# Kernel tuning notes

Hardware: AMD Instinct MI355X
Metric: run time of the kernel (lower is better)

The kernel has to match this reference:

```python
import jax, jax.numpy as jnp
import numpy as np

EMB = 128  # embsize
WORD = 128  # word_size
ITERS = 2


def _agg(embeds, neibors):
    # embeds: [B, N, D], neibors: [B, N, K] indices into node axis N (per batch)
    # mean-pool gathered neighbor embeddings -> [B, N, D]
    gathered = jax.vmap(lambda e, idx: e[idx])(embeds, neibors)  # [B, N, K, D]
    return gathered.mean(axis=2)


def setup_inputs() -> dict:
    key = jax.random.key(0)
    ks = jax.random.split(key, 9)
    B, N, K = 64, 512, 16
    word_embs = jax.random.normal(ks[0], (B, N, WORD), dtype=jnp.float32)
    lib_embs = jax.random.normal(ks[1], (B, N, WORD), dtype=jnp.float32)
    neibors = jax.random.randint(ks[2], (B, N, K), 0, N)
    neibors_lib = jax.random.randint(ks[3], (B, N, K), 0, N)
    mask = jax.random.uniform(ks[4], (B, N), dtype=jnp.float32)
    # xavier-uniform style params
    def xav(k, shape):
        bound = float(np.sqrt(6.0 / (shape[0] + shape[1])))
        return jax.random.uniform(k, shape, dtype=jnp.float32, minval=-bound, maxval=bound)
    weight = xav(ks[5], (WORD, EMB))
    weight2 = xav(ks[6], (EMB, EMB))
    enc_w1 = xav(ks[7], (WORD, EMB))
    enc_w2 = xav(ks[8], (EMB, EMB))
    return {"word_embs": word_embs, "neibors": neibors, "lib_embs": lib_embs,
            "neibors_lib": neibors_lib, "mask": mask, "weight": weight,
            "weight2": weight2, "enc_w1": enc_w1, "enc_w2": enc_w2}


def reference(word_embs, neibors, lib_embs, neibors_lib, mask, weight, weight2, enc_w1, enc_w2):
    B, N, _ = word_embs.shape
    # lib aggregation is loop-invariant (lib_embs fixed); same math as in-loop recompute
    agg_lib = jnp.einsum('bnw,we->bne', _agg(lib_embs, neibors_lib), weight)  # [B, N, EMB]
    word_proj = jnp.einsum('bnw,we->bne', word_embs, enc_w1)  # loop-invariant
    last_embed = jnp.zeros((B, N, EMB), dtype=jnp.float32)
    for _ in range(ITERS):
        agg_func = _agg(last_embed, neibors)  # [B, N, EMB]
        last_embed = jnp.tanh(word_proj + jnp.einsum('bne,ef->bnf', agg_func, enc_w2) + agg_lib)
    # masked sum over nodes, then final linear
    pooled = (last_embed * mask[:, :, None]).sum(axis=1)  # [B, EMB]
    return pooled @ weight2
```

## Files before the change

### kernel.cpp

```cpp
#include <hip/hip_runtime.h>
#include <hip/hip_bf16.h>

#define B_   64
#define N_   512
#define D_   128
#define NPB  16
#define G1   ((B_*N_)/NPB)

typedef float f32x4  __attribute__((ext_vector_type(4)));
typedef _Float16 f16x8 __attribute__((ext_vector_type(8)));

static __device__ __forceinline__ unsigned pkrtz(float x, float y) {
    return __builtin_bit_cast(unsigned, __builtin_amdgcn_cvt_pkrtz(x, y));
}
static __device__ __forceinline__ short f2h(float x) {
    _Float16 h = (_Float16)x;
    return __builtin_bit_cast(short, h);
}
static __device__ __forceinline__ float h2f(short s) {
    return (float)__builtin_bit_cast(_Float16, s);
}
static __device__ __forceinline__ float fast_tanh(float x) {
    float e = __expf(2.f * x);
    return 1.f - 2.f * __builtin_amdgcn_rcpf(e + 1.f);
}
static __device__ __forceinline__ void pk_add16(unsigned& acc, unsigned v) {
    asm("v_pk_add_f16 %0, %1, %0" : "+v"(acc) : "v"(v));
}

__global__ __launch_bounds__(256) void prep(const float* __restrict__ lib,
                                            const float* __restrict__ enc1,
                                            const float* __restrict__ wgt,
                                            const float* __restrict__ enc2,
                                            short* __restrict__ libh,
                                            short* __restrict__ Bp1,
                                            short* __restrict__ Bp2,
                                            float* __restrict__ out) {
    const int blk = blockIdx.x;
    if (blk < 1024) {
        const size_t g = ((size_t)blk * 256 + threadIdx.x) * 16;
        unsigned o[8];
#pragma unroll
        for (int q = 0; q < 4; ++q) {
            float4 v = *(const float4*)&lib[g + q * 4];
            o[q * 2]     = pkrtz(v.x, v.y);
            o[q * 2 + 1] = pkrtz(v.z, v.w);
        }
        *(int4*)&libh[g]     = *(int4*)o;
        *(int4*)&libh[g + 8] = *(int4*)(o + 4);
        return;
    }
    int tid = (blk - 1024) * 256 + threadIdx.x;
    out[tid] = 0.f;
    short o8[8];
    if (tid < 4096) {
        int l = tid & 63, nt = (tid >> 6) & 7, ks = tid >> 9;
        int k0 = ks * 32 + (l >> 4) * 8;
        int col = nt * 16 + (l & 15);
#pragma unroll
        for (int j = 0; j < 8; ++j) {
            int r = k0 + j;
            float v = (r < 128) ? enc1[r * 128 + col] : wgt[(r - 128) * 128 + col] * 0.0625f;
            o8[j] = f2h(v);
        }
        *(int4*)&Bp1[(size_t)tid * 8] = *(int4*)o8;
    } else if (tid < 6144) {
        int t2 = tid - 4096;
        int l = t2 & 63, nt = (t2 >> 6) & 7, ks = t2 >> 9;
        int k0 = ks * 32 + (l >> 4) * 8;
        int col = nt * 16 + (l & 15);
#pragma unroll
        for (int j = 0; j < 8; ++j) o8[j] = f2h(enc2[(k0 + j) * 128 + col] * 0.0625f);
        *(int4*)&Bp2[(size_t)t2 * 8] = *(int4*)o8;
    }
}

static __device__ __forceinline__ int swz_blk() {
    const int hw = blockIdx.x;
    return ((hw & 7) << 8) + (hw >> 3);
}

#define LDA1 264
#define LDA2 136

__global__ __launch_bounds__(256) void gemm1(const float* __restrict__ word,
                                             const int* __restrict__ nbrL,
                                             const short* __restrict__ libh,
                                             const short* __restrict__ Bp1,
                                             short* __restrict__ baseh,
                                             short* __restrict__ t1) {
    __shared__ short sA[NPB * LDA1];
    __shared__ int sIdx[NPB * 16];
    const int tid = threadIdx.x;
    const int blk = swz_blk();
    const int b = blk >> 5;
    const int node0 = blk * NPB;

    if (tid < 64) *(int4*)&sIdx[tid * 4] = *(const int4*)&nbrL[(size_t)node0 * 16 + tid * 4];
    __syncthreads();

    const int row = tid >> 4;
    const int lg  = tid & 15;

    {
        const float* wr = word + (size_t)(node0 + row) * D_ + lg * 8;
        float4 v0 = *(const float4*)&wr[0];
        float4 v1 = *(const float4*)&wr[4];
        unsigned o[4] = { pkrtz(v0.x, v0.y), pkrtz(v0.z, v0.w),
                          pkrtz(v1.x, v1.y), pkrtz(v1.z, v1.w) };
        *(int4*)&sA[row * LDA1 + lg * 8] = *(int4*)o;
    }

    {
        int idxr[16];
#pragma unroll
        for (int q = 0; q < 4; ++q) *(int4*)&idxr[q * 4] = *(const int4*)&sIdx[row * 16 + q * 4];
        const char* libB = (const char*)libh + (size_t)b * N_ * D_ * 2 + lg * 16;
        unsigned a0 = 0, a1 = 0, a2 = 0, a3 = 0;
#pragma unroll
        for (int nb = 0; nb < 16; ++nb) {
            int4 d = *(const int4*)(libB + ((unsigned)idxr[nb] << 8));
            pk_add16(a0, (unsigned)d.x);
            pk_add16(a1, (unsigned)d.y);
            pk_add16(a2, (unsigned)d.z);
            pk_add16(a3, (unsigned)d.w);
        }
        unsigned o[4] = { a0, a1, a2, a3 };
        *(int4*)&sA[row * LDA1 + 128 + lg * 8] = *(int4*)o;
    }
    __syncthreads();

    const int w = tid >> 6, l = tid & 63;
    f32x4 acc[2];
    acc[0] = (f32x4)0.f; acc[1] = (f32x4)0.f;
    const int arow = l & 15;
#pragma unroll
    for (int ks = 0; ks < 8; ++ks) {
        f16x8 a = *(const f16x8*)&sA[arow * LDA1 + ks * 32 + (l >> 4) * 8];
#pragma unroll
        for (int j = 0; j < 2; ++j) {
            const int nt = 2 * w + j;
            f16x8 bb = *(const f16x8*)&Bp1[((size_t)(ks * 8 + nt) * 64 + l) * 8];
            acc[j] = __builtin_amdgcn_mfma_f32_16x16x32_f16(a, bb, acc[j], 0, 0, 0);
        }
    }

    const int r0 = (l >> 4) * 4;
    const int cl = l & 15;
#pragma unroll
    for (int j = 0; j < 2; ++j) {
        const int col = (2 * w + j) * 16 + cl;
#pragma unroll
        for (int r = 0; r < 4; ++r) {
            size_t o = (size_t)(node0 + r0 + r) * D_ + col;
            float v = acc[j][r];
            baseh[o] = f2h(v);
            t1[o]    = f2h(fast_tanh(v));
        }
    }
}

__global__ __launch_bounds__(256) void gemm2(const short* __restrict__ t1,
                                             const int* __restrict__ nbr,
                                             const short* __restrict__ Bp2,
                                             const short* __restrict__ baseh,
                                             const float* __restrict__ mask,
                                             const float* __restrict__ w2,
                                             float* __restrict__ out) {
    __shared__ short sA[NPB * LDA2];
    __shared__ int sIdx[NPB * 16];
    __shared__ float pred[128];
    __shared__ float smask[NPB];
    const int tid = threadIdx.x;
    const int blk = swz_blk();
    const int b = blk >> 5;
    const int node0 = blk * NPB;

    if (tid < 64) *(int4*)&sIdx[tid * 4] = *(const int4*)&nbr[(size_t)node0 * 16 + tid * 4];
    if (tid >= 64 && tid < 64 + NPB) smask[tid - 64] = mask[node0 + tid - 64];
    __syncthreads();

    const int row = tid >> 4;
    const int lg  = tid & 15;
    {
        int idxr[16];
#pragma unroll
        for (int q = 0; q < 4; ++q) *(int4*)&idxr[q * 4] = *(const int4*)&sIdx[row * 16 + q * 4];
        const char* tB = (const char*)t1 + (size_t)b * N_ * D_ * 2 + lg * 16;
        unsigned a0 = 0, a1 = 0, a2 = 0, a3 = 0;
#pragma unroll
        for (int nb = 0; nb < 16; ++nb) {
            int4 d = *(const int4*)(tB + ((unsigned)idxr[nb] << 8));
            pk_add16(a0, (unsigned)d.x);
            pk_add16(a1, (unsigned)d.y);
            pk_add16(a2, (unsigned)d.z);
            pk_add16(a3, (unsigned)d.w);
        }
        unsigned o[4] = { a0, a1, a2, a3 };
        *(int4*)&sA[row * LDA2 + lg * 8] = *(int4*)o;
    }
    __syncthreads();

    const int w = tid >> 6, l = tid & 63;
    f32x4 acc[2];
    acc[0] = (f32x4)0.f; acc[1] = (f32x4)0.f;
    const int arow = l & 15;
#pragma unroll
    for (int ks = 0; ks < 4; ++ks) {
        f16x8 a = *(const f16x8*)&sA[arow * LDA2 + ks * 32 + (l >> 4) * 8];
#pragma unroll
        for (int j = 0; j < 2; ++j) {
            const int nt = 2 * w + j;
            f16x8 bb = *(const f16x8*)&Bp2[((size_t)(ks * 8 + nt) * 64 + l) * 8];
            acc[j] = __builtin_amdgcn_mfma_f32_16x16x32_f16(a, bb, acc[j], 0, 0, 0);
        }
    }

    const int r0 = (l >> 4) * 4;
    const int cl = l & 15;
#pragma unroll
    for (int j = 0; j < 2; ++j) {
        const int col = (2 * w + j) * 16 + cl;
        float s = 0.f;
#pragma unroll
        for (int r = 0; r < 4; ++r) {
            size_t o = (size_t)(node0 + r0 + r) * D_ + col;
            float v = fast_tanh(h2f(baseh[o]) + acc[j][r]);
            s += v * smask[r0 + r];
        }
        s += __shfl_xor(s, 16);
        s += __shfl_xor(s, 32);
        if (l < 16) pred[col] = s;
    }
    __syncthreads();
    if (tid < 128) {
        float a2 = 0.f;
#pragma unroll 4
        for (int f = 0; f < 128; ++f) a2 += pred[f] * w2[f * 128 + tid];
        atomicAdd(&out[b * 128 + tid], a2);
    }
}

extern "C" void kernel_launch(void* const* d_in, const int* in_sizes, int n_in,
                              void* d_out, int out_size, void* d_ws, size_t ws_size,
                              hipStream_t stream) {
    const float* word_embs   = (const float*)d_in[0];
    const int*   neibors     = (const int*)d_in[1];
    const float* lib_embs    = (const float*)d_in[2];
    const int*   neibors_lib = (const int*)d_in[3];
    const float* mask        = (const float*)d_in[4];
    const float* weight      = (const float*)d_in[5];
    const float* weight2     = (const float*)d_in[6];
    const float* enc_w1      = (const float*)d_in[7];
    const float* enc_w2      = (const float*)d_in[8];
    float* out = (float*)d_out;

    char* ws = (char*)d_ws;
    short* baseh = (short*)(ws);
    short* t1    = (short*)(ws + (1u << 23));
    short* libh  = (short*)(ws + (2u << 23));
    short* Bp1   = (short*)(ws + (3u << 23));
    short* Bp2   = (short*)(ws + (3u << 23) + 65536);

    prep<<<1056, 256, 0, stream>>>(lib_embs, enc_w1, weight, enc_w2, libh, Bp1, Bp2, out);
    gemm1<<<G1, 256, 0, stream>>>(word_embs, neibors_lib, libh, Bp1, baseh, t1);
    gemm2<<<G1, 256, 0, stream>>>(t1, neibors, Bp2, baseh, mask, weight2, out);
}
```

Before: 48.29 us.

## Reorder aggregation and matmul; gather neighbors from LDS windows in separate kernels

Neighbor mean-aggregation is linear, so the second-iteration matmul by enc_w2 is applied per node before aggregating. That lets the first kernel produce both the base projection and u = tanh(base)·W2. Neighbor gathers move into dedicated kernels (aggL, aggU). Each one loads a per-batch, per-16-channel slice of all 512 nodes into shared memory and gathers from there instead of doing random global loads. The lib embeddings are stored channel-chunked for contiguous slice loads, and a final kernel applies tanh, mask pooling and the weight2 projection. This trades fewer scattered global reads for two extra launches and extra intermediate buffers written and read through global memory.

```diff
diff --git a/kernel.cpp b/kernel.cpp
--- a/kernel.cpp
+++ b/kernel.cpp
@@ -4,8 +4,6 @@
 #define B_   64
 #define N_   512
 #define D_   128
-#define NPB  16
-#define G1   ((B_*N_)/NPB)
 
 typedef float f32x4  __attribute__((ext_vector_type(4)));
 typedef _Float16 f16x8 __attribute__((ext_vector_type(8)));
@@ -32,22 +30,26 @@
                                             const float* __restrict__ enc1,
                                             const float* __restrict__ wgt,
                                             const float* __restrict__ enc2,
-                                            short* __restrict__ libh,
+                                            short* __restrict__ libc,
                                             short* __restrict__ Bp1,
                                             short* __restrict__ Bp2,
                                             float* __restrict__ out) {
     const int blk = blockIdx.x;
     if (blk < 1024) {
-        const size_t g = ((size_t)blk * 256 + threadIdx.x) * 16;
+        const int g = blk * 256 + threadIdx.x;
+        const int b = g >> 12, rem = g & 4095;
+        const int r = rem >> 3, ch = rem & 7;
+        const float* src = lib + ((size_t)(b * 512 + r)) * 128 + ch * 16;
         unsigned o[8];
 #pragma unroll
         for (int q = 0; q < 4; ++q) {
-            float4 v = *(const float4*)&lib[g + q * 4];
+            float4 v = *(const float4*)&src[q * 4];
             o[q * 2]     = pkrtz(v.x, v.y);
             o[q * 2 + 1] = pkrtz(v.z, v.w);
         }
-        *(int4*)&libh[g]     = *(int4*)o;
-        *(int4*)&libh[g + 8] = *(int4*)(o + 4);
+        short* dst = libc + ((size_t)((b * 8 + ch) * 512 + r)) * 16;
+        *(int4*)&dst[0] = *(int4*)o;
+        *(int4*)&dst[8] = *(int4*)(o + 4);
         return;
     }
     int tid = (blk - 1024) * 256 + threadIdx.x;
@@ -75,65 +77,133 @@
     }
 }
 
-static __device__ __forceinline__ int swz_blk() {
+static __device__ __forceinline__ int swz512() {
+    const int hw = blockIdx.x;
+    return ((hw & 7) << 6) + (hw >> 3);
+}
+static __device__ __forceinline__ int swz2048() {
     const int hw = blockIdx.x;
     return ((hw & 7) << 8) + (hw >> 3);
 }
 
+#define WROW 40
+
+__global__ __launch_bounds__(256) void aggL(const short* __restrict__ libc,
+                                            const int* __restrict__ nbrL,
+                                            short* __restrict__ agg) {
+    __shared__ char win[512 * WROW];
+    const int t = threadIdx.x;
+    const int logical = swz512();
+    const int b = logical >> 3, ch = logical & 7;
+
+    const short* src = libc + (size_t)(b * 8 + ch) * 8192;
+#pragma unroll
+    for (int q = 0; q < 4; ++q) {
+        const int u = t + 256 * q;
+        int4 v = *(const int4*)&src[u * 8];
+        *(int4*)(win + (u >> 1) * WROW + (u & 1) * 16) = v;
+    }
+    __syncthreads();
+
+#pragma unroll
+    for (int rr = 0; rr < 2; ++rr) {
+        const int row = t * 2 + rr;
+        int idx[16];
+#pragma unroll
+        for (int q = 0; q < 4; ++q)
+            *(int4*)&idx[q * 4] = *(const int4*)&nbrL[(size_t)(b * 512 + row) * 16 + q * 4];
+#pragma unroll
+        for (int half = 0; half < 2; ++half) {
+            unsigned a0 = 0, a1 = 0, a2 = 0, a3 = 0;
+#pragma unroll
+            for (int nb = 0; nb < 16; ++nb) {
+                int4 d = *(const int4*)(win + idx[nb] * WROW + half * 16);
+                pk_add16(a0, (unsigned)d.x);
+                pk_add16(a1, (unsigned)d.y);
+                pk_add16(a2, (unsigned)d.z);
+                pk_add16(a3, (unsigned)d.w);
+            }
+            unsigned o[4] = { a0, a1, a2, a3 };
+            *(int4*)&agg[(size_t)(b * 512 + row) * 128 + ch * 16 + half * 8] = *(int4*)o;
+        }
+    }
+}
+
+__global__ __launch_bounds__(256) void aggU(const short* __restrict__ u,
+                                            const int* __restrict__ nbr,
+                                            short* __restrict__ aggu) {
+    __shared__ char win[512 * WROW];
+    const int t = threadIdx.x;
+    const int logical = swz512();
+    const int b = logical >> 3, ch = logical & 7;
+
+#pragma unroll
+    for (int q = 0; q < 4; ++q) {
+        const int uu = t + 256 * q;
+        int4 v = *(const int4*)&u[(size_t)(b * 512 + (uu >> 1)) * 128 + ch * 16 + (uu & 1) * 8];
+        *(int4*)(win + (uu >> 1) * WROW + (uu & 1) * 16) = v;
+    }
+    __syncthreads();
+
+#pragma unroll
+    for (int rr = 0; rr < 2; ++rr) {
+        const int row = t * 2 + rr;
+        int idx[16];
+#pragma unroll
+        for (int q = 0; q < 4; ++q)
+            *(int4*)&idx[q * 4] = *(const int4*)&nbr[(size_t)(b * 512 + row) * 16 + q * 4];
+#pragma unroll
+        for (int half = 0; half < 2; ++half) {
+            unsigned a0 = 0, a1 = 0, a2 = 0, a3 = 0;
+#pragma unroll
+            for (int nb = 0; nb < 16; ++nb) {
+                int4 d = *(const int4*)(win + idx[nb] * WROW + half * 16);
+                pk_add16(a0, (unsigned)d.x);
+                pk_add16(a1, (unsigned)d.y);
+                pk_add16(a2, (unsigned)d.z);
+                pk_add16(a3, (unsigned)d.w);
+            }
+            unsigned o[4] = { a0, a1, a2, a3 };
+            *(int4*)&aggu[(size_t)(b * 512 + row) * 128 + ch * 16 + half * 8] = *(int4*)o;
+        }
+    }
+}
+
 #define LDA1 264
 #define LDA2 136
 
-__global__ __launch_bounds__(256) void gemm1(const float* __restrict__ word,
-                                             const int* __restrict__ nbrL,
-                                             const short* __restrict__ libh,
-                                             const short* __restrict__ Bp1,
-                                             short* __restrict__ baseh,
-                                             short* __restrict__ t1) {
-    __shared__ short sA[NPB * LDA1];
-    __shared__ int sIdx[NPB * 16];
-    const int tid = threadIdx.x;
-    const int blk = swz_blk();
-    const int b = blk >> 5;
-    const int node0 = blk * NPB;
-
-    if (tid < 64) *(int4*)&sIdx[tid * 4] = *(const int4*)&nbrL[(size_t)node0 * 16 + tid * 4];
-    __syncthreads();
-
-    const int row = tid >> 4;
-    const int lg  = tid & 15;
+__global__ __launch_bounds__(256) void mm1(const float* __restrict__ word,
+                                           const short* __restrict__ agg,
+                                           const short* __restrict__ Bp1,
+                                           const short* __restrict__ Bp2,
+                                           short* __restrict__ baseh,
+                                           short* __restrict__ u) {
+    __shared__ short sA[16 * LDA1];
+    __shared__ short t1l[16 * LDA2];
+    __shared__ short obuf[16 * 128];
+    const int t = threadIdx.x;
+    const int blk = swz2048();
+    const int node0 = blk * 16;
 
     {
+        const int row = t >> 4, lg = t & 15;
         const float* wr = word + (size_t)(node0 + row) * D_ + lg * 8;
         float4 v0 = *(const float4*)&wr[0];
         float4 v1 = *(const float4*)&wr[4];
         unsigned o[4] = { pkrtz(v0.x, v0.y), pkrtz(v0.z, v0.w),
                           pkrtz(v1.x, v1.y), pkrtz(v1.z, v1.w) };
         *(int4*)&sA[row * LDA1 + lg * 8] = *(int4*)o;
-    }
-
-    {
-        int idxr[16];
-#pragma unroll
-        for (int q = 0; q < 4; ++q) *(int4*)&idxr[q * 4] = *(const int4*)&sIdx[row * 16 + q * 4];
-        const char* libB = (const char*)libh + (size_t)b * N_ * D_ * 2 + lg * 16;
-        unsigned a0 = 0, a1 = 0, a2 = 0, a3 = 0;
-#pragma unroll
-        for (int nb = 0; nb < 16; ++nb) {
-            int4 d = *(const int4*)(libB + ((unsigned)idxr[nb] << 8));
-            pk_add16(a0, (unsigned)d.x);
-            pk_add16(a1, (unsigned)d.y);
-            pk_add16(a2, (unsigned)d.z);
-            pk_add16(a3, (unsigned)d.w);
-        }
-        unsigned o[4] = { a0, a1, a2, a3 };
-        *(int4*)&sA[row * LDA1 + 128 + lg * 8] = *(int4*)o;
-    }
-    __syncthreads();
-
-    const int w = tid >> 6, l = tid & 63;
+        int4 av = *(const int4*)&agg[(size_t)(node0 + row) * D_ + lg * 8];
+        *(int4*)&sA[row * LDA1 + 128 + lg * 8] = av;
+    }
+    __syncthreads();
+
+    const int w = t >> 6, l = t & 63;
+    const int arow = l & 15;
+    const int r0 = (l >> 4) * 4, cl = l & 15;
+
     f32x4 acc[2];
     acc[0] = (f32x4)0.f; acc[1] = (f32x4)0.f;
-    const int arow = l & 15;
 #pragma unroll
     for (int ks = 0; ks < 8; ++ks) {
         f16x8 a = *(const f16x8*)&sA[arow * LDA1 + ks * 32 + (l >> 4) * 8];
@@ -145,99 +215,93 @@
         }
     }
 
-    const int r0 = (l >> 4) * 4;
-    const int cl = l & 15;
 #pragma unroll
     for (int j = 0; j < 2; ++j) {
         const int col = (2 * w + j) * 16 + cl;
 #pragma unroll
         for (int r = 0; r < 4; ++r) {
-            size_t o = (size_t)(node0 + r0 + r) * D_ + col;
             float v = acc[j][r];
-            baseh[o] = f2h(v);
-            t1[o]    = f2h(fast_tanh(v));
-        }
-    }
-}
-
-__global__ __launch_bounds__(256) void gemm2(const short* __restrict__ t1,
-                                             const int* __restrict__ nbr,
-                                             const short* __restrict__ Bp2,
-                                             const short* __restrict__ baseh,
-                                             const float* __restrict__ mask,
-                                             const float* __restrict__ w2,
-                                             float* __restrict__ out) {
-    __shared__ short sA[NPB * LDA2];
-    __shared__ int sIdx[NPB * 16];
-    __shared__ float pred[128];
-    __shared__ float smask[NPB];
-    const int tid = threadIdx.x;
-    const int blk = swz_blk();
-    const int b = blk >> 5;
-    const int node0 = blk * NPB;
-
-    if (tid < 64) *(int4*)&sIdx[tid * 4] = *(const int4*)&nbr[(size_t)node0 * 16 + tid * 4];
-    if (tid >= 64 && tid < 64 + NPB) smask[tid - 64] = mask[node0 + tid - 64];
-    __syncthreads();
-
-    const int row = tid >> 4;
-    const int lg  = tid & 15;
-    {
-        int idxr[16];
-#pragma unroll
-        for (int q = 0; q < 4; ++q) *(int4*)&idxr[q * 4] = *(const int4*)&sIdx[row * 16 + q * 4];
-        const char* tB = (const char*)t1 + (size_t)b * N_ * D_ * 2 + lg * 16;
-        unsigned a0 = 0, a1 = 0, a2 = 0, a3 = 0;
-#pragma unroll
-        for (int nb = 0; nb < 16; ++nb) {
-            int4 d = *(const int4*)(tB + ((unsigned)idxr[nb] << 8));
-            pk_add16(a0, (unsigned)d.x);
-            pk_add16(a1, (unsigned)d.y);
-            pk_add16(a2, (unsigned)d.z);
-            pk_add16(a3, (unsigned)d.w);
-        }
-        unsigned o[4] = { a0, a1, a2, a3 };
-        *(int4*)&sA[row * LDA2 + lg * 8] = *(int4*)o;
-    }
-    __syncthreads();
-
-    const int w = tid >> 6, l = tid & 63;
-    f32x4 acc[2];
-    acc[0] = (f32x4)0.f; acc[1] = (f32x4)0.f;
-    const int arow = l & 15;
+            obuf[(r0 + r) * 128 + col] = f2h(v);
+            t1l[(r0 + r) * LDA2 + col] = f2h(fast_tanh(v));
+        }
+    }
+    __syncthreads();
+    *(int4*)&baseh[(size_t)node0 * 128 + t * 8] = *(const int4*)&obuf[t * 8];
+
+    f32x4 a2[2];
+    a2[0] = (f32x4)0.f; a2[1] = (f32x4)0.f;
 #pragma unroll
     for (int ks = 0; ks < 4; ++ks) {
-        f16x8 a = *(const f16x8*)&sA[arow * LDA2 + ks * 32 + (l >> 4) * 8];
+        f16x8 a = *(const f16x8*)&t1l[arow * LDA2 + ks * 32 + (l >> 4) * 8];
 #pragma unroll
         for (int j = 0; j < 2; ++j) {
             const int nt = 2 * w + j;
             f16x8 bb = *(const f16x8*)&Bp2[((size_t)(ks * 8 + nt) * 64 + l) * 8];
-            acc[j] = __builtin_amdgcn_mfma_f32_16x16x32_f16(a, bb, acc[j], 0, 0, 0);
-        }
-    }
-
-    const int r0 = (l >> 4) * 4;
-    const int cl = l & 15;
+            a2[j] = __builtin_amdgcn_mfma_f32_16x16x32_f16(a, bb, a2[j], 0, 0, 0);
+        }
+    }
+    __syncthreads();
 #pragma unroll
     for (int j = 0; j < 2; ++j) {
         const int col = (2 * w + j) * 16 + cl;
-        float s = 0.f;
-#pragma unroll
-        for (int r = 0; r < 4; ++r) {
-            size_t o = (size_t)(node0 + r0 + r) * D_ + col;
-            float v = fast_tanh(h2f(baseh[o]) + acc[j][r]);
-            s += v * smask[r0 + r];
-        }
-        s += __shfl_xor(s, 16);
-        s += __shfl_xor(s, 32);
-        if (l < 16) pred[col] = s;
-    }
-    __syncthreads();
-    if (tid < 128) {
+#pragma unroll
+        for (int r = 0; r < 4; ++r)
+            obuf[(r0 + r) * 128 + col] = f2h(a2[j][r]);
+    }
+    __syncthreads();
+    *(int4*)&u[(size_t)node0 * 128 + t * 8] = *(const int4*)&obuf[t * 8];
+}
+
+__global__ __launch_bounds__(256) void fin(const short* __restrict__ baseh,
+                                           const short* __restrict__ aggu,
+                                           const float* __restrict__ mask,
+                                           const float* __restrict__ w2,
+                                           float* __restrict__ out) {
+    __shared__ float pred[8 * 128];
+    __shared__ float tot[128];
+    __shared__ float smask[64];
+    const int t = threadIdx.x;
+    const int logical = swz512();
+    const int b = logical >> 3, g = logical & 7;
+    const int node0 = b * 512 + g * 64;
+
+    if (t < 64) smask[t] = mask[node0 + t];
+    __syncthreads();
+
+    const int c4 = (t & 31) * 4;
+    const int rg = t >> 5;
+    float s0 = 0.f, s1 = 0.f, s2 = 0.f, s3 = 0.f;
+#pragma unroll
+    for (int i = 0; i < 8; ++i) {
+        const int r = rg * 8 + i;
+        const size_t o = (size_t)(node0 + r) * 128 + c4;
+        uint2 bv = *(const uint2*)&baseh[o];
+        uint2 av = *(const uint2*)&aggu[o];
+        const short* bs = (const short*)&bv;
+        const short* as = (const short*)&av;
+        const float mk = smask[r];
+        s0 += mk * fast_tanh(h2f(bs[0]) + h2f(as[0]));
+        s1 += mk * fast_tanh(h2f(bs[1]) + h2f(as[1]));
+        s2 += mk * fast_tanh(h2f(bs[2]) + h2f(as[2]));
+        s3 += mk * fast_tanh(h2f(bs[3]) + h2f(as[3]));
+    }
+    pred[rg * 128 + c4 + 0] = s0;
+    pred[rg * 128 + c4 + 1] = s1;
+    pred[rg * 128 + c4 + 2] = s2;
+    pred[rg * 128 + c4 + 3] = s3;
+    __syncthreads();
+    if (t < 128) {
+        float tt = 0.f;
+#pragma unroll
+        for (int i = 0; i < 8; ++i) tt += pred[i * 128 + t];
+        tot[t] = tt;
+    }
+    __syncthreads();
+    if (t < 128) {
         float a2 = 0.f;
 #pragma unroll 4
-        for (int f = 0; f < 128; ++f) a2 += pred[f] * w2[f * 128 + tid];
-        atomicAdd(&out[b * 128 + tid], a2);
+        for (int f = 0; f < 128; ++f) a2 += tot[f] * w2[f * 128 + t];
+        atomicAdd(&out[b * 128 + t], a2);
     }
 }
 
@@ -257,12 +321,16 @@
 
     char* ws = (char*)d_ws;
     short* baseh = (short*)(ws);
-    short* t1    = (short*)(ws + (1u << 23));
-    short* libh  = (short*)(ws + (2u << 23));
-    short* Bp1   = (short*)(ws + (3u << 23));
-    short* Bp2   = (short*)(ws + (3u << 23) + 65536);
-
-    prep<<<1056, 256, 0, stream>>>(lib_embs, enc_w1, weight, enc_w2, libh, Bp1, Bp2, out);
-    gemm1<<<G1, 256, 0, stream>>>(word_embs, neibors_lib, libh, Bp1, baseh, t1);
-    gemm2<<<G1, 256, 0, stream>>>(t1, neibors, Bp2, baseh, mask, weight2, out);
-}
+    short* ubuf  = (short*)(ws + (1u << 23));
+    short* libc  = (short*)(ws + (2u << 23));
+    short* aggb  = (short*)(ws + (3u << 23));
+    short* aggu  = (short*)(ws + (4u << 23));
+    short* Bp1   = (short*)(ws + (5u << 23));
+    short* Bp2   = (short*)(ws + (5u << 23) + 65536);
+
+    prep<<<1056, 256, 0, stream>>>(lib_embs, enc_w1, weight, enc_w2, libc, Bp1, Bp2, out);
+    aggL<<<512, 256, 0, stream>>>(libc, neibors_lib, aggb);
+    mm1<<<2048, 256, 0, stream>>>(word_embs, aggb, Bp1, Bp2, baseh, ubuf);
+    aggU<<<512, 256, 0, stream>>>(ubuf, neibors, aggu);
+    fin<<<512, 256, 0, stream>>>(baseh, aggu, mask, weight2, out);
+}
```

Result: slower. 61.13 us (+26.6%).
